# Performance work log

Hardware: AMD Instinct MI355X
Metric: run time of the kernel (lower is better)

The kernel has to match this reference:

```python
import jax, jax.numpy as jnp
import numpy as np

N_NODES = 100000
N_EDGES = 3200000
D_FEAT = 128


def setup_inputs() -> dict:
    key = jax.random.key(0)
    k1, k2, k3, k4 = jax.random.split(key, 4)
    rows = jax.random.randint(k1, (N_EDGES,), 0, N_NODES, dtype=jnp.int32)
    cols = jax.random.randint(k2, (N_EDGES,), 0, N_NODES, dtype=jnp.int32)
    vals = jax.random.uniform(k3, (N_EDGES,), dtype=jnp.float32)
    embeds = jax.random.normal(k4, (N_NODES, D_FEAT), dtype=jnp.float32)
    return {"rows": rows, "cols": cols, "vals": vals, "embeds": embeds}


def reference(rows, cols, vals, embeds):
    # out = adj @ embeds, adj in COO form: out[r] += vals[e] * embeds[cols[e]]
    gathered = vals[:, None] * embeds[cols]          # [E, D]
    out = jax.ops.segment_sum(gathered, rows, num_segments=N_NODES)  # [N, D]
    return out
```

## Files before the change

### kernel.cpp

```cpp
#include <hip/hip_runtime.h>

#define D_FEAT  128
#define RSHIFT  6
#define RPB     64
#define NB_MAX  2048
#define NBLK    256
#define P2T     512
#define P2CAP   12544
#define BT      256
#define CAP     2432

#define CHSHIFT 13
#define NCH     16
#define SBINS   (RPB * NCH)

__global__ void zero_out_kernel(float* __restrict__ out, int n4) {
    int i = blockIdx.x * blockDim.x + threadIdx.x;
    if (i < n4) ((float4*)out)[i] = make_float4(0.f, 0.f, 0.f, 0.f);
}

__global__ void coo_scatter_atomic_kernel(const int* __restrict__ rows,
                                          const int* __restrict__ cols,
                                          const float* __restrict__ vals,
                                          const float* __restrict__ embeds,
                                          float* __restrict__ out,
                                          int n_edges) {
    int tid  = blockIdx.x * blockDim.x + threadIdx.x;
    int edge = tid >> 5;
    int lane = tid & 31;
    if (edge >= n_edges) return;
    int   r = rows[edge];
    int   c = cols[edge];
    float v = vals[edge];
    const float4* src = (const float4*)(embeds + (size_t)c * D_FEAT);
    float4 e = src[lane];
    float* dst = out + (size_t)r * D_FEAT + lane * 4;
    atomicAdd(dst + 0, v * e.x);
    atomicAdd(dst + 1, v * e.y);
    atomicAdd(dst + 2, v * e.z);
    atomicAdd(dst + 3, v * e.w);
}

__device__ inline unsigned short f2bf(float f) {
    unsigned int u = __float_as_uint(f);
    u += 0x7fffu + ((u >> 16) & 1u);
    return (unsigned short)(u >> 16);
}

__global__ __launch_bounds__(256) void conv_bf16_pack_kernel(const float* __restrict__ in,
                                                             uint2* __restrict__ out,
                                                             int n_nodes) {
    int tid = blockIdx.x * blockDim.x + threadIdx.x;
    int c = tid >> 5, l = tid & 31;
    if (c >= n_nodes) return;
    float4 f = ((const float4*)(in + (size_t)c * D_FEAT))[l];
    uint2 q;
    q.x = (unsigned)f2bf(f.x) | ((unsigned)f2bf(f.y) << 16);
    q.y = (unsigned)f2bf(f.z) | ((unsigned)f2bf(f.w) << 16);
    out[(size_t)c * 32 + l] = q;
}


__global__ __launch_bounds__(P2T) void p1_count(const int* __restrict__ rows,
                                                int* __restrict__ Cmat,
                                                int n_edges, int nb, int tile) {
    __shared__ int cnt[NB_MAX];
    int blk = blockIdx.x, t = threadIdx.x;
    for (int b = t; b < nb; b += P2T) cnt[b] = 0;
    __syncthreads();
    int e0 = blk * tile;
    int e1 = min(e0 + tile, n_edges);
    for (int i = e0 + t; i < e1; i += P2T)
        atomicAdd(&cnt[rows[i] >> RSHIFT], 1);
    __syncthreads();
    int* dst = Cmat + (size_t)blk * nb;
    for (int b = t; b < nb; b += P2T) dst[b] = cnt[b];
}

__global__ __launch_bounds__(NBLK) void s3_fused(const int* __restrict__ Cmat,
                                                 int* __restrict__ BmatT,
                                                 int* __restrict__ total, int nb) {
    __shared__ int s[NBLK];
    int b = blockIdx.x, t = threadIdx.x;
    int v = Cmat[(size_t)t * nb + b];
    s[t] = v;
    __syncthreads();
    for (int off = 1; off < NBLK; off <<= 1) {
        int u = (t >= off) ? s[t - off] : 0;
        __syncthreads();
        s[t] += u;
        __syncthreads();
    }
    BmatT[(size_t)b * NBLK + t] = s[t] - v;
    if (t == NBLK - 1) total[b] = s[t];
}

__global__ __launch_bounds__(1024) void s2_base(const int* __restrict__ total,
                                                int* __restrict__ base, int nb) {
    __shared__ int s[2048];
    int t = threadIdx.x;
    int v0 = (t < nb) ? total[t] : 0;
    int v1 = (t + 1024 < nb) ? total[t + 1024] : 0;
    s[t] = v0;
    s[t + 1024] = v1;
    __syncthreads();
    for (int off = 1; off < 2048; off <<= 1) {
        int u0 = (t >= off) ? s[t - off] : 0;
        int u1 = (t + 1024 >= off) ? s[t + 1024 - off] : 0;
        __syncthreads();
        s[t] += u0;
        s[t + 1024] += u1;
        __syncthreads();
    }
    if (t < nb)        base[t]        = s[t]        - v0;
    if (t + 1024 < nb) base[t + 1024] = s[t + 1024] - v1;
}

__global__ __launch_bounds__(P2T) void p2_scatter(const int* __restrict__ rows,
                                                  const int* __restrict__ cols,
                                                  const float* __restrict__ vals,
                                                  const int* __restrict__ base,
                                                  const int* __restrict__ BmatT,
                                                  const int* __restrict__ Cmat,
                                                  int2* __restrict__ pairs,
                                                  int n_edges, int nb, int tile) {
    __shared__ int2           stage[P2CAP];
    __shared__ unsigned short bkt[P2CAP];
    __shared__ int            lcur[NB_MAX];
    __shared__ int            goff[NB_MAX];
    __shared__ int            scan_s[P2T];

    int blk = blockIdx.x, t = threadIdx.x;

    const int* crow = Cmat + (size_t)blk * nb;
    int b0 = t << 2;
    int c0 = (b0     < nb) ? crow[b0]     : 0;
    int c1 = (b0 + 1 < nb) ? crow[b0 + 1] : 0;
    int c2 = (b0 + 2 < nb) ? crow[b0 + 2] : 0;
    int c3 = (b0 + 3 < nb) ? crow[b0 + 3] : 0;
    int local = c0 + c1 + c2 + c3;
    scan_s[t] = local;
    __syncthreads();
    for (int off = 1; off < P2T; off <<= 1) {
        int u = (t >= off) ? scan_s[t - off] : 0;
        __syncthreads();
        scan_s[t] += u;
        __syncthreads();
    }
    int e = scan_s[t] - local;
    if (b0     < nb) { lcur[b0]     = e; goff[b0]     = base[b0]     + BmatT[(size_t)(b0)     * NBLK + blk] - e; }
    e += c0;
    if (b0 + 1 < nb) { lcur[b0 + 1] = e; goff[b0 + 1] = base[b0 + 1] + BmatT[(size_t)(b0 + 1) * NBLK + blk] - e; }
    e += c1;
    if (b0 + 2 < nb) { lcur[b0 + 2] = e; goff[b0 + 2] = base[b0 + 2] + BmatT[(size_t)(b0 + 2) * NBLK + blk] - e; }
    e += c2;
    if (b0 + 3 < nb) { lcur[b0 + 3] = e; goff[b0 + 3] = base[b0 + 3] + BmatT[(size_t)(b0 + 3) * NBLK + blk] - e; }
    __syncthreads();

    int e0 = blk * tile;
    int e1 = min(e0 + tile, n_edges);
    int ntile = e1 - e0;
    for (int i = e0 + t; i < e1; i += P2T) {
        int   r = rows[i];
        int   c = cols[i];
        float v = vals[i];
        int   b = r >> RSHIFT;
        int pos = atomicAdd(&lcur[b], 1);
        stage[pos] = make_int2(c | ((r & (RPB - 1)) << 17), __float_as_int(v));
        bkt[pos]   = (unsigned short)b;
    }
    __syncthreads();

    for (int i = t; i < ntile; i += P2T) {
        int b = bkt[i];
        pairs[goff[b] + i] = stage[i];
    }
}

__global__ __launch_bounds__(256) void sort_bucket_kernel(const int* __restrict__ total,
                                                          const int* __restrict__ base,
                                                          int2* __restrict__ pairs,
                                                          int* __restrict__ rowbeg,
                                                          int* __restrict__ rowend,
                                                          int n_rows) {
    __shared__ int2 stage[CAP];
    __shared__ int  hist[SBINS];
    __shared__ int  ex[SBINS + 1];
    __shared__ int  scan_s[256];

    int b = blockIdx.x, t = threadIdx.x;
    int n     = total[b];
    int pbase = base[b];
    if (n > CAP) n = CAP;

    for (int i = t; i < SBINS; i += 256) hist[i] = 0;
    __syncthreads();
    for (int i = t; i < n; i += 256) {
        int x = pairs[pbase + i].x;
        int key = (((x >> 17) & (RPB - 1)) << 4) | ((x >> CHSHIFT) & (NCH - 1));
        atomicAdd(&hist[key], 1);
    }
    __syncthreads();
    int h0 = hist[4 * t], h1 = hist[4 * t + 1], h2 = hist[4 * t + 2], h3 = hist[4 * t + 3];
    int local = h0 + h1 + h2 + h3;
    scan_s[t] = local;
    __syncthreads();
    for (int off = 1; off < 256; off <<= 1) {
        int u = (t >= off) ? scan_s[t - off] : 0;
        __syncthreads();
        scan_s[t] += u;
        __syncthreads();
    }
    int bt = scan_s[t] - local;
    ex[4 * t]     = bt;
    ex[4 * t + 1] = bt + h0;
    ex[4 * t + 2] = bt + h0 + h1;
    ex[4 * t + 3] = bt + h0 + h1 + h2;
    hist[4 * t]     = bt;
    hist[4 * t + 1] = bt + h0;
    hist[4 * t + 2] = bt + h0 + h1;
    hist[4 * t + 3] = bt + h0 + h1 + h2;
    if (t == 255) ex[SBINS] = bt + local;
    __syncthreads();

    for (int i = t; i < n; i += 256) {
        int2 p  = pairs[pbase + i];
        int key = (((p.x >> 17) & (RPB - 1)) << 4) | ((p.x >> CHSHIFT) & (NCH - 1));
        int pos = atomicAdd(&hist[key], 1);
        stage[pos] = make_int2(p.x & 0x1FFFF, p.y);
    }
    __syncthreads();

    for (int i = t; i < n; i += 256) pairs[pbase + i] = stage[i];
    if (t < RPB) {
        int row = (b << RSHIFT) + t;
        if (row < n_rows) {
            rowbeg[row] = pbase + ex[t << 4];
            rowend[row] = pbase + ex[(t + 1) << 4];
        }
    }
}

template <bool BF16>
__global__ __launch_bounds__(256, 4) void reduce_row_kernel(const int* __restrict__ rowbeg,
                                                            const int* __restrict__ rowend,
                                                            const int2* __restrict__ pairs,
                                                            const float* __restrict__ embF,
                                                            const uint2* __restrict__ embB,
                                                            float* __restrict__ out,
                                                            int n_rows) {
    int g    = threadIdx.x >> 5;
    int lane = threadIdx.x & 31;
    int row  = (blockIdx.x << 3) + g;
    if (row >= n_rows) return;
    int s0 = rowbeg[row];
    int s1 = rowend[row];
    float4 acc = make_float4(0.f, 0.f, 0.f, 0.f);

    int i = s0;
    for (; i + 7 < s1; i += 8) {
        int2 p0 = pairs[i + 0], p1 = pairs[i + 1], p2 = pairs[i + 2], p3 = pairs[i + 3];
        int2 p4 = pairs[i + 4], p5 = pairs[i + 5], p6 = pairs[i + 6], p7 = pairs[i + 7];
        if (BF16) {
            uint2 q0 = embB[(size_t)p0.x * 32 + lane];
            uint2 q1 = embB[(size_t)p1.x * 32 + lane];
            uint2 q2 = embB[(size_t)p2.x * 32 + lane];
            uint2 q3 = embB[(size_t)p3.x * 32 + lane];
            uint2 q4 = embB[(size_t)p4.x * 32 + lane];
            uint2 q5 = embB[(size_t)p5.x * 32 + lane];
            uint2 q6 = embB[(size_t)p6.x * 32 + lane];
            uint2 q7 = embB[(size_t)p7.x * 32 + lane];
#define ACC(pp, qq) {                                                        \
            float v = __int_as_float((pp).y);                                \
            acc.x += v * __uint_as_float((qq).x << 16);                      \
            acc.y += v * __uint_as_float((qq).x & 0xffff0000u);              \
            acc.z += v * __uint_as_float((qq).y << 16);                      \
            acc.w += v * __uint_as_float((qq).y & 0xffff0000u); }
            ACC(p0, q0); ACC(p1, q1); ACC(p2, q2); ACC(p3, q3);
            ACC(p4, q4); ACC(p5, q5); ACC(p6, q6); ACC(p7, q7);
#undef ACC
        } else {
            const float4* e4 = (const float4*)embF;
            float4 q0 = e4[(size_t)p0.x * 32 + lane];
            float4 q1 = e4[(size_t)p1.x * 32 + lane];
            float4 q2 = e4[(size_t)p2.x * 32 + lane];
            float4 q3 = e4[(size_t)p3.x * 32 + lane];
            float4 q4 = e4[(size_t)p4.x * 32 + lane];
            float4 q5 = e4[(size_t)p5.x * 32 + lane];
            float4 q6 = e4[(size_t)p6.x * 32 + lane];
            float4 q7 = e4[(size_t)p7.x * 32 + lane];
#define ACCF(pp, qq) {                                                       \
            float v = __int_as_float((pp).y);                                \
            acc.x += v * (qq).x; acc.y += v * (qq).y;                        \
            acc.z += v * (qq).z; acc.w += v * (qq).w; }
            ACCF(p0, q0); ACCF(p1, q1); ACCF(p2, q2); ACCF(p3, q3);
            ACCF(p4, q4); ACCF(p5, q5); ACCF(p6, q6); ACCF(p7, q7);
#undef ACCF
        }
    }
    for (; i < s1; ++i) {
        int2 p = pairs[i];
        float v = __int_as_float(p.y);
        if (BF16) {
            uint2 q = embB[(size_t)p.x * 32 + lane];
            acc.x += v * __uint_as_float(q.x << 16);
            acc.y += v * __uint_as_float(q.x & 0xffff0000u);
            acc.z += v * __uint_as_float(q.y << 16);
            acc.w += v * __uint_as_float(q.y & 0xffff0000u);
        } else {
            float4 q = ((const float4*)embF)[(size_t)p.x * 32 + lane];
            acc.x += v * q.x; acc.y += v * q.y; acc.z += v * q.z; acc.w += v * q.w;
        }
    }
    ((float4*)(out + (size_t)row * D_FEAT))[lane] = acc;
}

extern "C" void kernel_launch(void* const* d_in, const int* in_sizes, int n_in,
                              void* d_out, int out_size, void* d_ws, size_t ws_size,
                              hipStream_t stream) {
    const int*   rows   = (const int*)d_in[0];
    const int*   cols   = (const int*)d_in[1];
    const float* vals   = (const float*)d_in[2];
    const float* embeds = (const float*)d_in[3];
    float*       out    = (float*)d_out;

    const int n_edges = in_sizes[0];
    const int n_rows  = out_size / D_FEAT;
    const int n_nodes = in_sizes[3] / D_FEAT;

    const int nb   = (n_rows + RPB - 1) >> RSHIFT;
    const int tile = (n_edges + NBLK - 1) / NBLK;

    size_t cmat_b  = (((size_t)NBLK * nb * sizeof(int)) + 255) & ~(size_t)255;
    size_t bmatT_b = (((size_t)nb * NBLK * sizeof(int)) + 255) & ~(size_t)255;
    size_t tot_b   = (((size_t)nb * sizeof(int)) + 255) & ~(size_t)255;
    size_t base_b  = tot_b;
    size_t pair_b  = (((size_t)n_edges * sizeof(int2)) + 255) & ~(size_t)255;
    size_t rbeg_b  = (((size_t)n_rows * sizeof(int)) + 255) & ~(size_t)255;
    size_t rend_b  = rbeg_b;
    size_t embB_b  = (size_t)n_nodes * D_FEAT * sizeof(unsigned short);
    size_t need0   = cmat_b + bmatT_b + tot_b + base_b + pair_b + rbeg_b + rend_b;
    size_t need1   = need0 + embB_b;

    bool ok = (ws_size >= need0) && (nb <= NB_MAX) && (tile <= P2CAP) &&
              (n_nodes <= (1 << 17)) && (n_rows <= (1 << 17));
    if (!ok) {
        int out_n4 = out_size / 4;
        zero_out_kernel<<<(out_n4 + 255) / 256, 256, 0, stream>>>(out, out_n4);
        long long totalT = (long long)n_edges * 32;
        int grid = (int)((totalT + 255) / 256);
        coo_scatter_atomic_kernel<<<grid, 256, 0, stream>>>(rows, cols, vals, embeds, out, n_edges);
        return;
    }
    bool use_bf16 = (ws_size >= need1);

    char* ws = (char*)d_ws;
    int*   Cmat   = (int*)ws;    ws += cmat_b;
    int*   BmatT  = (int*)ws;    ws += bmatT_b;
    int*   total  = (int*)ws;    ws += tot_b;
    int*   base   = (int*)ws;    ws += base_b;
    int2*  pairs  = (int2*)ws;   ws += pair_b;
    int*   rowbeg = (int*)ws;    ws += rbeg_b;
    int*   rowend = (int*)ws;    ws += rend_b;
    uint2* embB   = (uint2*)ws;

    if (use_bf16) {
        int nthreads = n_nodes * 32;
        conv_bf16_pack_kernel<<<(nthreads + 255) / 256, 256, 0, stream>>>(embeds, embB, n_nodes);
    }
    p1_count  <<<NBLK, P2T,  0, stream>>>(rows, Cmat, n_edges, nb, tile);
    s3_fused  <<<nb,   NBLK, 0, stream>>>(Cmat, BmatT, total, nb);
    s2_base   <<<1,    1024, 0, stream>>>(total, base, nb);
    p2_scatter<<<NBLK, P2T,  0, stream>>>(rows, cols, vals, base, BmatT, Cmat, pairs,
                                          n_edges, nb, tile);
    sort_bucket_kernel<<<nb, 256, 0, stream>>>(total, base, pairs, rowbeg, rowend, n_rows);

    int rgrid = (n_rows + 7) / 8;
    if (use_bf16)
        reduce_row_kernel<true><<<rgrid, 256, 0, stream>>>(rowbeg, rowend, pairs,
                                                           embeds, embB, out, n_rows);
    else
        reduce_row_kernel<false><<<rgrid, 256, 0, stream>>>(rowbeg, rowend, pairs,
                                                            embeds, embB, out, n_rows);
}
```

Baseline: 302.0 us.

## Fuse bucket sort with row reduction and replace base scan with atomic offsets

The per-bucket sort and the row reduction now run in one kernel, which reads the sorted (col,val) pairs from LDS instead of writing them back to global memory and launching a separate reduce kernel. The secondary column-chunk sort key is dropped, so the sort only groups edges by row. The single-block base scan is replaced by an atomicAdd on a global counter inside s3_fused, which removes one launch but makes bucket placement order nondeterministic. The fused kernel has far fewer blocks (one per 64 rows) and holds a large LDS stage buffer, so occupancy and latency hiding of the gathers may fall, and column locality inside each row is lost.

```diff
diff --git a/kernel.cpp b/kernel.cpp
--- a/kernel.cpp
+++ b/kernel.cpp
@@ -7,12 +7,7 @@
 #define NBLK    256
 #define P2T     512
 #define P2CAP   12544
-#define BT      256
 #define CAP     2432
-
-#define CHSHIFT 13
-#define NCH     16
-#define SBINS   (RPB * NCH)
 
 __global__ void zero_out_kernel(float* __restrict__ out, int n4) {
     int i = blockIdx.x * blockDim.x + threadIdx.x;
@@ -63,9 +58,11 @@
 
 __global__ __launch_bounds__(P2T) void p1_count(const int* __restrict__ rows,
                                                 int* __restrict__ Cmat,
+                                                int* __restrict__ counter,
                                                 int n_edges, int nb, int tile) {
     __shared__ int cnt[NB_MAX];
     int blk = blockIdx.x, t = threadIdx.x;
+    if (blk == 0 && t == 0) *counter = 0;
     for (int b = t; b < nb; b += P2T) cnt[b] = 0;
     __syncthreads();
     int e0 = blk * tile;
@@ -79,7 +76,9 @@
 
 __global__ __launch_bounds__(NBLK) void s3_fused(const int* __restrict__ Cmat,
                                                  int* __restrict__ BmatT,
-                                                 int* __restrict__ total, int nb) {
+                                                 int* __restrict__ total,
+                                                 int* __restrict__ base,
+                                                 int* __restrict__ counter, int nb) {
     __shared__ int s[NBLK];
     int b = blockIdx.x, t = threadIdx.x;
     int v = Cmat[(size_t)t * nb + b];
@@ -92,28 +91,10 @@
         __syncthreads();
     }
     BmatT[(size_t)b * NBLK + t] = s[t] - v;
-    if (t == NBLK - 1) total[b] = s[t];
-}
-
-__global__ __launch_bounds__(1024) void s2_base(const int* __restrict__ total,
-                                                int* __restrict__ base, int nb) {
-    __shared__ int s[2048];
-    int t = threadIdx.x;
-    int v0 = (t < nb) ? total[t] : 0;
-    int v1 = (t + 1024 < nb) ? total[t + 1024] : 0;
-    s[t] = v0;
-    s[t + 1024] = v1;
-    __syncthreads();
-    for (int off = 1; off < 2048; off <<= 1) {
-        int u0 = (t >= off) ? s[t - off] : 0;
-        int u1 = (t + 1024 >= off) ? s[t + 1024 - off] : 0;
-        __syncthreads();
-        s[t] += u0;
-        s[t + 1024] += u1;
-        __syncthreads();
-    }
-    if (t < nb)        base[t]        = s[t]        - v0;
-    if (t + 1024 < nb) base[t + 1024] = s[t + 1024] - v1;
+    if (t == NBLK - 1) {
+        total[b] = s[t];
+        base[b]  = atomicAdd(counter, s[t]);
+    }
 }
 
 __global__ __launch_bounds__(P2T) void p2_scatter(const int* __restrict__ rows,
@@ -177,142 +158,114 @@
     }
 }
 
-__global__ __launch_bounds__(256) void sort_bucket_kernel(const int* __restrict__ total,
+template <bool BF16>
+__global__ __launch_bounds__(256) void sort_reduce_kernel(const int* __restrict__ total,
                                                           const int* __restrict__ base,
-                                                          int2* __restrict__ pairs,
-                                                          int* __restrict__ rowbeg,
-                                                          int* __restrict__ rowend,
+                                                          const int2* __restrict__ pairs,
+                                                          const float* __restrict__ embF,
+                                                          const uint2* __restrict__ embB,
+                                                          float* __restrict__ out,
                                                           int n_rows) {
     __shared__ int2 stage[CAP];
-    __shared__ int  hist[SBINS];
-    __shared__ int  ex[SBINS + 1];
-    __shared__ int  scan_s[256];
+    __shared__ int  hist[RPB];
+    __shared__ int  ex[RPB + 1];
 
     int b = blockIdx.x, t = threadIdx.x;
     int n     = total[b];
     int pbase = base[b];
     if (n > CAP) n = CAP;
 
-    for (int i = t; i < SBINS; i += 256) hist[i] = 0;
-    __syncthreads();
-    for (int i = t; i < n; i += 256) {
-        int x = pairs[pbase + i].x;
-        int key = (((x >> 17) & (RPB - 1)) << 4) | ((x >> CHSHIFT) & (NCH - 1));
-        atomicAdd(&hist[key], 1);
-    }
-    __syncthreads();
-    int h0 = hist[4 * t], h1 = hist[4 * t + 1], h2 = hist[4 * t + 2], h3 = hist[4 * t + 3];
-    int local = h0 + h1 + h2 + h3;
-    scan_s[t] = local;
-    __syncthreads();
-    for (int off = 1; off < 256; off <<= 1) {
-        int u = (t >= off) ? scan_s[t - off] : 0;
-        __syncthreads();
-        scan_s[t] += u;
-        __syncthreads();
-    }
-    int bt = scan_s[t] - local;
-    ex[4 * t]     = bt;
-    ex[4 * t + 1] = bt + h0;
-    ex[4 * t + 2] = bt + h0 + h1;
-    ex[4 * t + 3] = bt + h0 + h1 + h2;
-    hist[4 * t]     = bt;
-    hist[4 * t + 1] = bt + h0;
-    hist[4 * t + 2] = bt + h0 + h1;
-    hist[4 * t + 3] = bt + h0 + h1 + h2;
-    if (t == 255) ex[SBINS] = bt + local;
+    if (t < RPB) hist[t] = 0;
+    __syncthreads();
+    for (int i = t; i < n; i += 256)
+        atomicAdd(&hist[(pairs[pbase + i].x >> 17) & (RPB - 1)], 1);
+    __syncthreads();
+    int hv = (t < RPB) ? hist[t] : 0;
+    if (t < RPB) ex[t + 1] = hv;
+    if (t == 0) ex[0] = 0;
+    __syncthreads();
+    for (int off = 1; off < RPB; off <<= 1) {
+        int u = (t < RPB && t >= off) ? ex[t + 1 - off] : 0;
+        __syncthreads();
+        if (t < RPB) ex[t + 1] += u;
+        __syncthreads();
+    }
+    if (t < RPB) hist[t] = ex[t + 1] - hv;
     __syncthreads();
 
     for (int i = t; i < n; i += 256) {
         int2 p  = pairs[pbase + i];
-        int key = (((p.x >> 17) & (RPB - 1)) << 4) | ((p.x >> CHSHIFT) & (NCH - 1));
-        int pos = atomicAdd(&hist[key], 1);
+        int  lr = (p.x >> 17) & (RPB - 1);
+        int pos = atomicAdd(&hist[lr], 1);
         stage[pos] = make_int2(p.x & 0x1FFFF, p.y);
     }
     __syncthreads();
 
-    for (int i = t; i < n; i += 256) pairs[pbase + i] = stage[i];
-    if (t < RPB) {
-        int row = (b << RSHIFT) + t;
-        if (row < n_rows) {
-            rowbeg[row] = pbase + ex[t << 4];
-            rowend[row] = pbase + ex[(t + 1) << 4];
+    int g    = t >> 5;
+    int lane = t & 31;
+    int row0 = b << RSHIFT;
+    for (int r = g; r < RPB; r += 8) {
+        int row = row0 + r;
+        if (row >= n_rows) break;
+        int s0 = ex[r], s1 = ex[r + 1];
+        float4 acc = make_float4(0.f, 0.f, 0.f, 0.f);
+        int i = s0;
+        for (; i + 7 < s1; i += 8) {
+            int2 p0 = stage[i + 0], p1 = stage[i + 1], p2 = stage[i + 2], p3 = stage[i + 3];
+            int2 p4 = stage[i + 4], p5 = stage[i + 5], p6 = stage[i + 6], p7 = stage[i + 7];
+            if (BF16) {
+                uint2 q0 = embB[(size_t)p0.x * 32 + lane];
+                uint2 q1 = embB[(size_t)p1.x * 32 + lane];
+                uint2 q2 = embB[(size_t)p2.x * 32 + lane];
+                uint2 q3 = embB[(size_t)p3.x * 32 + lane];
+                uint2 q4 = embB[(size_t)p4.x * 32 + lane];
+                uint2 q5 = embB[(size_t)p5.x * 32 + lane];
+                uint2 q6 = embB[(size_t)p6.x * 32 + lane];
+                uint2 q7 = embB[(size_t)p7.x * 32 + lane];
+#define ACC(pp, qq) {                                                        \
+                float v = __int_as_float((pp).y);                            \
+                acc.x += v * __uint_as_float((qq).x << 16);                  \
+                acc.y += v * __uint_as_float((qq).x & 0xffff0000u);          \
+                acc.z += v * __uint_as_float((qq).y << 16);                  \
+                acc.w += v * __uint_as_float((qq).y & 0xffff0000u); }
+                ACC(p0, q0); ACC(p1, q1); ACC(p2, q2); ACC(p3, q3);
+                ACC(p4, q4); ACC(p5, q5); ACC(p6, q6); ACC(p7, q7);
+#undef ACC
+            } else {
+                const float4* e4 = (const float4*)embF;
+                float4 q0 = e4[(size_t)p0.x * 32 + lane];
+                float4 q1 = e4[(size_t)p1.x * 32 + lane];
+                float4 q2 = e4[(size_t)p2.x * 32 + lane];
+                float4 q3 = e4[(size_t)p3.x * 32 + lane];
+                float4 q4 = e4[(size_t)p4.x * 32 + lane];
+                float4 q5 = e4[(size_t)p5.x * 32 + lane];
+                float4 q6 = e4[(size_t)p6.x * 32 + lane];
+                float4 q7 = e4[(size_t)p7.x * 32 + lane];
+#define ACCF(pp, qq) {                                                       \
+                float v = __int_as_float((pp).y);                            \
+                acc.x += v * (qq).x; acc.y += v * (qq).y;                    \
+                acc.z += v * (qq).z; acc.w += v * (qq).w; }
+                ACCF(p0, q0); ACCF(p1, q1); ACCF(p2, q2); ACCF(p3, q3);
+                ACCF(p4, q4); ACCF(p5, q5); ACCF(p6, q6); ACCF(p7, q7);
+#undef ACCF
+            }
         }
-    }
-}
-
-template <bool BF16>
-__global__ __launch_bounds__(256, 4) void reduce_row_kernel(const int* __restrict__ rowbeg,
-                                                            const int* __restrict__ rowend,
-                                                            const int2* __restrict__ pairs,
-                                                            const float* __restrict__ embF,
-                                                            const uint2* __restrict__ embB,
-                                                            float* __restrict__ out,
-                                                            int n_rows) {
-    int g    = threadIdx.x >> 5;
-    int lane = threadIdx.x & 31;
-    int row  = (blockIdx.x << 3) + g;
-    if (row >= n_rows) return;
-    int s0 = rowbeg[row];
-    int s1 = rowend[row];
-    float4 acc = make_float4(0.f, 0.f, 0.f, 0.f);
-
-    int i = s0;
-    for (; i + 7 < s1; i += 8) {
-        int2 p0 = pairs[i + 0], p1 = pairs[i + 1], p2 = pairs[i + 2], p3 = pairs[i + 3];
-        int2 p4 = pairs[i + 4], p5 = pairs[i + 5], p6 = pairs[i + 6], p7 = pairs[i + 7];
-        if (BF16) {
-            uint2 q0 = embB[(size_t)p0.x * 32 + lane];
-            uint2 q1 = embB[(size_t)p1.x * 32 + lane];
-            uint2 q2 = embB[(size_t)p2.x * 32 + lane];
-            uint2 q3 = embB[(size_t)p3.x * 32 + lane];
-            uint2 q4 = embB[(size_t)p4.x * 32 + lane];
-            uint2 q5 = embB[(size_t)p5.x * 32 + lane];
-            uint2 q6 = embB[(size_t)p6.x * 32 + lane];
-            uint2 q7 = embB[(size_t)p7.x * 32 + lane];
-#define ACC(pp, qq) {                                                        \
-            float v = __int_as_float((pp).y);                                \
-            acc.x += v * __uint_as_float((qq).x << 16);                      \
-            acc.y += v * __uint_as_float((qq).x & 0xffff0000u);              \
-            acc.z += v * __uint_as_float((qq).y << 16);                      \
-            acc.w += v * __uint_as_float((qq).y & 0xffff0000u); }
-            ACC(p0, q0); ACC(p1, q1); ACC(p2, q2); ACC(p3, q3);
-            ACC(p4, q4); ACC(p5, q5); ACC(p6, q6); ACC(p7, q7);
-#undef ACC
-        } else {
-            const float4* e4 = (const float4*)embF;
-            float4 q0 = e4[(size_t)p0.x * 32 + lane];
-            float4 q1 = e4[(size_t)p1.x * 32 + lane];
-            float4 q2 = e4[(size_t)p2.x * 32 + lane];
-            float4 q3 = e4[(size_t)p3.x * 32 + lane];
-            float4 q4 = e4[(size_t)p4.x * 32 + lane];
-            float4 q5 = e4[(size_t)p5.x * 32 + lane];
-            float4 q6 = e4[(size_t)p6.x * 32 + lane];
-            float4 q7 = e4[(size_t)p7.x * 32 + lane];
-#define ACCF(pp, qq) {                                                       \
-            float v = __int_as_float((pp).y);                                \
-            acc.x += v * (qq).x; acc.y += v * (qq).y;                        \
-            acc.z += v * (qq).z; acc.w += v * (qq).w; }
-            ACCF(p0, q0); ACCF(p1, q1); ACCF(p2, q2); ACCF(p3, q3);
-            ACCF(p4, q4); ACCF(p5, q5); ACCF(p6, q6); ACCF(p7, q7);
-#undef ACCF
+        for (; i < s1; ++i) {
+            int2 p = stage[i];
+            float v = __int_as_float(p.y);
+            if (BF16) {
+                uint2 q = embB[(size_t)p.x * 32 + lane];
+                acc.x += v * __uint_as_float(q.x << 16);
+                acc.y += v * __uint_as_float(q.x & 0xffff0000u);
+                acc.z += v * __uint_as_float(q.y << 16);
+                acc.w += v * __uint_as_float(q.y & 0xffff0000u);
+            } else {
+                float4 q = ((const float4*)embF)[(size_t)p.x * 32 + lane];
+                acc.x += v * q.x; acc.y += v * q.y; acc.z += v * q.z; acc.w += v * q.w;
+            }
         }
-    }
-    for (; i < s1; ++i) {
-        int2 p = pairs[i];
-        float v = __int_as_float(p.y);
-        if (BF16) {
-            uint2 q = embB[(size_t)p.x * 32 + lane];
-            acc.x += v * __uint_as_float(q.x << 16);
-            acc.y += v * __uint_as_float(q.x & 0xffff0000u);
-            acc.z += v * __uint_as_float(q.y << 16);
-            acc.w += v * __uint_as_float(q.y & 0xffff0000u);
-        } else {
-            float4 q = ((const float4*)embF)[(size_t)p.x * 32 + lane];
-            acc.x += v * q.x; acc.y += v * q.y; acc.z += v * q.z; acc.w += v * q.w;
-        }
-    }
-    ((float4*)(out + (size_t)row * D_FEAT))[lane] = acc;
+        ((float4*)(out + (size_t)row * D_FEAT))[lane] = acc;
+    }
 }
 
 extern "C" void kernel_launch(void* const* d_in, const int* in_sizes, int n_in,
@@ -335,11 +288,10 @@
     size_t bmatT_b = (((size_t)nb * NBLK * sizeof(int)) + 255) & ~(size_t)255;
     size_t tot_b   = (((size_t)nb * sizeof(int)) + 255) & ~(size_t)255;
     size_t base_b  = tot_b;
+    size_t ctr_b   = 256;
     size_t pair_b  = (((size_t)n_edges * sizeof(int2)) + 255) & ~(size_t)255;
-    size_t rbeg_b  = (((size_t)n_rows * sizeof(int)) + 255) & ~(size_t)255;
-    size_t rend_b  = rbeg_b;
     size_t embB_b  = (size_t)n_nodes * D_FEAT * sizeof(unsigned short);
-    size_t need0   = cmat_b + bmatT_b + tot_b + base_b + pair_b + rbeg_b + rend_b;
+    size_t need0   = cmat_b + bmatT_b + tot_b + base_b + ctr_b + pair_b;
     size_t need1   = need0 + embB_b;
 
     bool ok = (ws_size >= need0) && (nb <= NB_MAX) && (tile <= P2CAP) &&
@@ -355,31 +307,26 @@
     bool use_bf16 = (ws_size >= need1);
 
     char* ws = (char*)d_ws;
-    int*   Cmat   = (int*)ws;    ws += cmat_b;
-    int*   BmatT  = (int*)ws;    ws += bmatT_b;
-    int*   total  = (int*)ws;    ws += tot_b;
-    int*   base   = (int*)ws;    ws += base_b;
-    int2*  pairs  = (int2*)ws;   ws += pair_b;
-    int*   rowbeg = (int*)ws;    ws += rbeg_b;
-    int*   rowend = (int*)ws;    ws += rend_b;
-    uint2* embB   = (uint2*)ws;
+    int*   Cmat    = (int*)ws;    ws += cmat_b;
+    int*   BmatT   = (int*)ws;    ws += bmatT_b;
+    int*   total   = (int*)ws;    ws += tot_b;
+    int*   base    = (int*)ws;    ws += base_b;
+    int*   counter = (int*)ws;    ws += ctr_b;
+    int2*  pairs   = (int2*)ws;   ws += pair_b;
+    uint2* embB    = (uint2*)ws;
 
     if (use_bf16) {
         int nthreads = n_nodes * 32;
         conv_bf16_pack_kernel<<<(nthreads + 255) / 256, 256, 0, stream>>>(embeds, embB, n_nodes);
     }
-    p1_count  <<<NBLK, P2T,  0, stream>>>(rows, Cmat, n_edges, nb, tile);
-    s3_fused  <<<nb,   NBLK, 0, stream>>>(Cmat, BmatT, total, nb);
-    s2_base   <<<1,    1024, 0, stream>>>(total, base, nb);
+    p1_count  <<<NBLK, P2T,  0, stream>>>(rows, Cmat, counter, n_edges, nb, tile);
+    s3_fused  <<<nb,   NBLK, 0, stream>>>(Cmat, BmatT, total, base, counter, nb);
     p2_scatter<<<NBLK, P2T,  0, stream>>>(rows, cols, vals, base, BmatT, Cmat, pairs,
                                           n_edges, nb, tile);
-    sort_bucket_kernel<<<nb, 256, 0, stream>>>(total, base, pairs, rowbeg, rowend, n_rows);
-
-    int rgrid = (n_rows + 7) / 8;
     if (use_bf16)
-        reduce_row_kernel<true><<<rgrid, 256, 0, stream>>>(rowbeg, rowend, pairs,
-                                                           embeds, embB, out, n_rows);
+        sort_reduce_kernel<true><<<nb, 256, 0, stream>>>(total, base, pairs,
+                                                         embeds, embB, out, n_rows);
     else
-        reduce_row_kernel<false><<<rgrid, 256, 0, stream>>>(rowbeg, rowend, pairs,
-                                                            embeds, embB, out, n_rows);
-}
+        sort_reduce_kernel<false><<<nb, 256, 0, stream>>>(total, base, pairs,
+                                                          embeds, embB, out, n_rows);
+}
```

Result: no change. 306.4 us (+1.5%).
